# Kernel optimization log

Measured on AMD Instinct MI355X. Metric: run time of the kernel, lower is better.

The kernel has to match this reference:

```python
import jax, jax.numpy as jnp
import numpy as np

B, N_IN, N_H, N_OUT = 128, 256, 256, 256


def _bimul(W, X):
    # MatrixBiMul: bilinear map W X W^T, W: [out, in], X: [b, in, in] -> [b, out, out]
    return jnp.einsum('oi,bij,qj->boq', W, X, W)


def setup_inputs() -> dict:
    key = jax.random.key(0)
    ks = jax.random.split(key, 12)
    s_in = 1.0 / np.sqrt(N_IN)
    s_h = 1.0 / np.sqrt(N_H)
    return {
        'input': jax.random.normal(ks[0], (B, N_IN, N_IN), jnp.float32),
        'hidden': jax.random.normal(ks[1], (B, N_H, N_H), jnp.float32),
        'cell': jax.random.normal(ks[2], (B, N_H, N_H), jnp.float32),
        'W_fx': jax.random.normal(ks[3], (N_H, N_IN), jnp.float32) * s_in,
        'W_ix': jax.random.normal(ks[4], (N_H, N_IN), jnp.float32) * s_in,
        'W_ox': jax.random.normal(ks[5], (N_OUT, N_IN), jnp.float32) * s_in,
        'W_gx': jax.random.normal(ks[6], (N_H, N_IN), jnp.float32) * s_in,
        'W_fh': jax.random.normal(ks[7], (N_H, N_H), jnp.float32) * s_h,
        'W_ih': jax.random.normal(ks[8], (N_H, N_H), jnp.float32) * s_h,
        'W_oh': jax.random.normal(ks[9], (N_OUT, N_H), jnp.float32) * s_h,
        'W_gh': jax.random.normal(ks[10], (N_H, N_H), jnp.float32) * s_h,
        'W_oc': jax.random.normal(ks[11], (N_OUT, N_H), jnp.float32) * s_h,
    }


def reference(input, hidden, cell, W_fx, W_ix, W_ox, W_gx, W_fh, W_ih, W_oh, W_gh, W_oc):
    fgate = jax.nn.relu(_bimul(W_fx, input) + _bimul(W_fh, hidden))
    igate = jax.nn.relu(_bimul(W_ix, input) + _bimul(W_ih, hidden))
    ogate = jax.nn.relu(_bimul(W_ox, input) + _bimul(W_oh, hidden))
    ggate = jax.nn.relu(_bimul(W_gx, input) + _bimul(W_gh, hidden))
    c = fgate + cell + igate + ggate  # note: additive, as in source (not fgate*cell)
    h = ogate + jax.nn.relu(_bimul(W_oc, c))
    return (h, c)
```

## Files before the change

### kernel.cpp

```cpp
#include <hip/hip_runtime.h>

typedef __bf16 bf16x8 __attribute__((ext_vector_type(8)));
typedef float f32x4 __attribute__((ext_vector_type(4)));

__device__ __forceinline__ unsigned short f2bf(float f) {
    unsigned int u = __builtin_bit_cast(unsigned int, f);
    u += 0x7fff + ((u >> 16) & 1);
    return (unsigned short)(u >> 16);
}

__device__ __forceinline__ void stage_tile(
    const unsigned short* __restrict__ Ap, int lda,
    const unsigned short* __restrict__ Bp, int ldb,
    unsigned short* lds, int k0, int tid)
{
#pragma unroll
    for (int it = 0; it < 4; ++it) {
        int li = it * 256 + tid;
        int row = li >> 3;
        int sc = ((li & 7) ^ (row & 7)) * 8;
        __builtin_amdgcn_global_load_lds(
            (const __attribute__((address_space(1))) void*)(Ap + (long)row * lda + k0 + sc),
            (__attribute__((address_space(3))) void*)&lds[li * 8], 16, 0, 0);
        __builtin_amdgcn_global_load_lds(
            (const __attribute__((address_space(1))) void*)(Bp + (long)row * ldb + k0 + sc),
            (__attribute__((address_space(3))) void*)&lds[8192 + li * 8], 16, 0, 0);
    }
}

__device__ __forceinline__ void compute_tile(
    const unsigned short* lds, int lane, int wm, int wn, f32x4 (&acc)[4][4])
{
#pragma unroll
    for (int kk = 0; kk < 2; ++kk) {
        const int cl = kk * 4 + (lane >> 4);
        bf16x8 af[4], bfr[4];
#pragma unroll
        for (int m = 0; m < 4; ++m) {
            int row = wm + m * 16 + (lane & 15);
            af[m] = *(const bf16x8*)&lds[row * 64 + ((cl ^ (row & 7)) * 8)];
        }
#pragma unroll
        for (int n = 0; n < 4; ++n) {
            int row = wn + n * 16 + (lane & 15);
            bfr[n] = *(const bf16x8*)&lds[8192 + row * 64 + ((cl ^ (row & 7)) * 8)];
        }
#pragma unroll
        for (int m = 0; m < 4; ++m)
#pragma unroll
            for (int n = 0; n < 4; ++n)
                acc[m][n] = __builtin_amdgcn_mfma_f32_16x16x32_bf16(af[m], bfr[n], acc[m][n], 0, 0, 0);
    }
}

__global__ __launch_bounds__(256)
void transpose_cvt(const float* __restrict__ S0, unsigned short* __restrict__ D0,
                   const float* __restrict__ S1, unsigned short* __restrict__ D1)
{
    const float* S = blockIdx.z ? S1 : S0;
    unsigned short* D = blockIdx.z ? D1 : D0;
    const int b = blockIdx.y;
    const int t = blockIdx.x;
    const int r0 = (t >> 2) * 64;
    const int c0 = (t & 3) * 64;
    S += (long)b * 65536;
    D += (long)b * 65536;

    __shared__ float tile[64][65];
    const int tid = threadIdx.x;

#pragma unroll
    for (int it = 0; it < 4; ++it) {
        int r = it * 16 + (tid >> 4);
        int c = (tid & 15) * 4;
        float4 v = *(const float4*)&S[(long)(r0 + r) * 256 + c0 + c];
        tile[r][c + 0] = v.x; tile[r][c + 1] = v.y;
        tile[r][c + 2] = v.z; tile[r][c + 3] = v.w;
    }
    __syncthreads();
#pragma unroll
    for (int it = 0; it < 16; ++it) {
        int rr = it * 4 + (tid >> 6);
        int cc = tid & 63;
        D[(long)(c0 + rr) * 256 + r0 + cc] = f2bf(tile[cc][rr]);
    }
}

__global__ __launch_bounds__(256)
void cvt_weights(const float* __restrict__ fx, const float* __restrict__ ix,
                 const float* __restrict__ ox, const float* __restrict__ gx,
                 const float* __restrict__ fh, const float* __restrict__ ih,
                 const float* __restrict__ oh, const float* __restrict__ gh,
                 const float* __restrict__ oc,
                 unsigned short* __restrict__ Wcat, unsigned short* __restrict__ Wocb)
{
    int idx = blockIdx.x * 256 + threadIdx.x;
    if (idx < 524288) {
        int g = idx >> 17;
        int rem = idx & 131071;
        int q = rem >> 9;
        int j = rem & 511;
        const float* xs = (g == 0) ? fx : (g == 1) ? ix : (g == 2) ? ox : gx;
        const float* hs = (g == 0) ? fh : (g == 1) ? ih : (g == 2) ? oh : gh;
        float v = (j < 256) ? xs[q * 256 + j] : hs[q * 256 + (j - 256)];
        Wcat[idx] = f2bf(v);
    } else if (idx < 589824) {
        int k = idx - 524288;
        Wocb[k] = f2bf(oc[k]);
    }
}

__global__ __launch_bounds__(256)
void gemm_stageA(const unsigned short* __restrict__ Wcat,
                 const unsigned short* __restrict__ XbT,
                 const unsigned short* __restrict__ HbT,
                 unsigned short* __restrict__ Tcat)
{
    __shared__ alignas(16) unsigned short lds[32768];

    const int tid = threadIdx.x;
    const int lane = tid & 63;
    const int w = tid >> 6;

    int d = blockIdx.x + 4 * blockIdx.y + 512 * blockIdx.z;
    int swz = (d & 7) * 512 + (d >> 3);
    const int x = swz & 3;
    const int b = (swz >> 2) & 127;
    const int gz = swz >> 9;
    const int g = gz >> 1, hf = gz & 1;
    const int tm = (x >> 1) * 128;
    const int tn = (x & 1) * 128;
    const int wm = (w >> 1) * 64;
    const int wn = (w & 1) * 64;

    const unsigned short* Ap = Wcat + (long)g * 131072 + hf * 256 + (long)tm * 512;
    const unsigned short* Bp = (hf ? HbT : XbT) + (long)b * 65536 + (long)tn * 256;

    f32x4 acc[4][4];
#pragma unroll
    for (int m = 0; m < 4; ++m)
#pragma unroll
        for (int n = 0; n < 4; ++n)
            acc[m][n] = (f32x4){0.f, 0.f, 0.f, 0.f};

    stage_tile(Ap, 512, Bp, 256, lds, 0, tid);
    __syncthreads();
    int cur = 0;
    for (int t = 0; t < 4; ++t) {
        if (t + 1 < 4)
            stage_tile(Ap, 512, Bp, 256, lds + (cur ^ 1) * 16384, (t + 1) * 64, tid);
        compute_tile(lds + cur * 16384, lane, wm, wn, acc);
        __syncthreads();
        cur ^= 1;
    }

    unsigned short* C = Tcat + (long)g * 16777216 + (long)b * 131072 + hf * 256;
    const int r0 = (lane >> 4) * 4;
    const int c0 = lane & 15;
#pragma unroll
    for (int m = 0; m < 4; ++m)
#pragma unroll
        for (int n = 0; n < 4; ++n)
#pragma unroll
            for (int r = 0; r < 4; ++r) {
                int row = tm + wm + m * 16 + r0 + r;
                int col = tn + wn + n * 16 + c0;
                C[(long)row * 512 + col] = f2bf(acc[m][n][r]);
            }
}

__global__ __launch_bounds__(256)
void gemm_gateB(const unsigned short* __restrict__ Tcat,
                const unsigned short* __restrict__ Wcat,
                const float* __restrict__ cell,
                float* __restrict__ out_c, float* __restrict__ out_h,
                unsigned short* __restrict__ CbT)
{
    __shared__ alignas(16) unsigned short lds[32768];

    const int tid = threadIdx.x;
    const int lane = tid & 63;
    const int w = tid >> 6;
    const int zc = (blockIdx.z == 0);

    int orig = blockIdx.x + 4 * blockIdx.y;
    int swz = (orig & 7) * 64 + (orig >> 3);
    const int x = swz & 3;
    const int b = swz >> 2;
    const int tm = (x >> 1) * 128;
    const int tn = (x & 1) * 128;
    const int wm = (w >> 1) * 64;
    const int wn = (w & 1) * 64;

    const int nseg = zc ? 3 : 1;
    auto abase = [&](int seg) -> const unsigned short* {
        int gv = zc ? (seg + (seg >> 1)) : 2;
        return Tcat + (long)gv * 16777216 + (long)b * 131072 + (long)tm * 512;
    };
    auto bbase = [&](int seg) -> const unsigned short* {
        int gv = zc ? (seg + (seg >> 1)) : 2;
        return Wcat + (long)gv * 131072 + (long)tn * 512;
    };

    f32x4 accc[4][4];
#pragma unroll
    for (int m = 0; m < 4; ++m)
#pragma unroll
        for (int n = 0; n < 4; ++n)
            accc[m][n] = (f32x4){0.f, 0.f, 0.f, 0.f};

    stage_tile(abase(0), 512, bbase(0), 512, lds, 0, tid);
    __syncthreads();
    int cur = 0;
    const int nt = nseg * 8;
    for (int seg = 0; seg < nseg; ++seg) {
        f32x4 acc[4][4];
#pragma unroll
        for (int m = 0; m < 4; ++m)
#pragma unroll
            for (int n = 0; n < 4; ++n)
                acc[m][n] = (f32x4){0.f, 0.f, 0.f, 0.f};
        for (int ks = 0; ks < 8; ++ks) {
            int u = seg * 8 + ks;
            if (u + 1 < nt) {
                int s2 = (u + 1) >> 3;
                int k2 = ((u + 1) & 7) * 64;
                stage_tile(abase(s2), 512, bbase(s2), 512, lds + (cur ^ 1) * 16384, k2, tid);
            }
            compute_tile(lds + cur * 16384, lane, wm, wn, acc);
            __syncthreads();
            cur ^= 1;
        }
#pragma unroll
        for (int m = 0; m < 4; ++m)
#pragma unroll
            for (int n = 0; n < 4; ++n)
#pragma unroll
                for (int r = 0; r < 4; ++r) {
                    float v = acc[m][n][r];
                    accc[m][n][r] += (v > 0.f ? v : 0.f);
                }
    }

    const int r0 = (lane >> 4) * 4;
    const int c0 = lane & 15;
    if (zc) {
        unsigned short (*ldsT)[136] = (unsigned short(*)[136])lds;
        const float* cb = cell + (long)b * 65536;
        float* co = out_c + (long)b * 65536;
#pragma unroll
        for (int m = 0; m < 4; ++m)
#pragma unroll
            for (int n = 0; n < 4; ++n)
#pragma unroll
                for (int r = 0; r < 4; ++r) {
                    int row = wm + m * 16 + r0 + r;
                    int col = wn + n * 16 + c0;
                    float v = accc[m][n][r] + cb[(long)(tm + row) * 256 + tn + col];
                    co[(long)(tm + row) * 256 + tn + col] = v;
                    ldsT[col][row] = f2bf(v);
                }
        __syncthreads();
        unsigned short* cbt = CbT + (long)b * 65536;
#pragma unroll
        for (int it = 0; it < 8; ++it) {
            int idx = it * 256 + tid;
            int jj = idx >> 4;
            int ch = idx & 15;
            uint4 v = *(const uint4*)&ldsT[jj][ch * 8];
            *(uint4*)&cbt[(long)(tn + jj) * 256 + tm + ch * 8] = v;
        }
    } else {
        float* ho = out_h + (long)b * 65536;
#pragma unroll
        for (int m = 0; m < 4; ++m)
#pragma unroll
            for (int n = 0; n < 4; ++n)
#pragma unroll
                for (int r = 0; r < 4; ++r) {
                    int row = tm + wm + m * 16 + r0 + r;
                    int col = tn + wn + n * 16 + c0;
                    ho[(long)row * 256 + col] = accc[m][n][r];
                }
    }
}

template <int MODE>
__global__ __launch_bounds__(256)
void gemm_nt2(const unsigned short* __restrict__ A, int lda, long sAy,
              const unsigned short* __restrict__ B, int ldb, long sBy,
              void* __restrict__ Cv, int ldc, long sCy, int nt)
{
    __shared__ alignas(16) unsigned short lds[32768];

    const int tid = threadIdx.x;
    const int lane = tid & 63;
    const int w = tid >> 6;

    int orig = blockIdx.x + 4 * blockIdx.y;
    int swz = (orig & 7) * 64 + (orig >> 3);
    const int x = swz & 3;
    const int b = swz >> 2;
    const int tm = (x >> 1) * 128;
    const int tn = (x & 1) * 128;
    const int wm = (w >> 1) * 64;
    const int wn = (w & 1) * 64;

    const unsigned short* Ap = A + b * sAy + (long)tm * lda;
    const unsigned short* Bp = B + b * sBy + (long)tn * ldb;

    f32x4 acc[4][4];
#pragma unroll
    for (int m = 0; m < 4; ++m)
#pragma unroll
        for (int n = 0; n < 4; ++n)
            acc[m][n] = (f32x4){0.f, 0.f, 0.f, 0.f};

    stage_tile(Ap, lda, Bp, ldb, lds, 0, tid);
    __syncthreads();
    int cur = 0;
    for (int t = 0; t < nt; ++t) {
        if (t + 1 < nt)
            stage_tile(Ap, lda, Bp, ldb, lds + (cur ^ 1) * 16384, (t + 1) * 64, tid);
        compute_tile(lds + cur * 16384, lane, wm, wn, acc);
        __syncthreads();
        cur ^= 1;
    }

    const long coff = b * sCy;
    const int r0 = (lane >> 4) * 4;
    const int c0 = lane & 15;

    if (MODE == 0) {
        unsigned short* C = (unsigned short*)Cv + coff;
#pragma unroll
        for (int m = 0; m < 4; ++m)
#pragma unroll
            for (int n = 0; n < 4; ++n)
#pragma unroll
                for (int r = 0; r < 4; ++r) {
                    int row = tm + wm + m * 16 + r0 + r;
                    int col = tn + wn + n * 16 + c0;
                    C[(long)row * ldc + col] = f2bf(acc[m][n][r]);
                }
    } else {
        float* C = (float*)Cv + coff;
#pragma unroll
        for (int m = 0; m < 4; ++m)
#pragma unroll
            for (int n = 0; n < 4; ++n)
#pragma unroll
                for (int r = 0; r < 4; ++r) {
                    int row = tm + wm + m * 16 + r0 + r;
                    int col = tn + wn + n * 16 + c0;
                    long idx = (long)row * ldc + col;
                    float v = acc[m][n][r];
                    C[idx] += (v > 0.f ? v : 0.f);
                }
    }
}

extern "C" void kernel_launch(void* const* d_in, const int* in_sizes, int n_in,
                              void* d_out, int out_size, void* d_ws, size_t ws_size,
                              hipStream_t stream)
{
    (void)in_sizes; (void)n_in; (void)out_size; (void)ws_size;

    const float* X    = (const float*)d_in[0];
    const float* H    = (const float*)d_in[1];
    const float* cell = (const float*)d_in[2];
    const float* Wxp[4] = {(const float*)d_in[3], (const float*)d_in[4],
                           (const float*)d_in[5], (const float*)d_in[6]};
    const float* Whp[4] = {(const float*)d_in[7], (const float*)d_in[8],
                           (const float*)d_in[9], (const float*)d_in[10]};
    const float* Wocf = (const float*)d_in[11];

    float* out_h = (float*)d_out;
    float* out_c = out_h + 8388608;

    unsigned short* ws   = (unsigned short*)d_ws;
    unsigned short* XbT  = ws;
    unsigned short* HbT  = ws + 8388608;
    unsigned short* Wcat = ws + 16777216;
    unsigned short* Wocb = ws + 17301504;
    unsigned short* Tcat = ws + 17367040;
    unsigned short* CbT  = XbT;
    unsigned short* U    = HbT;

    transpose_cvt<<<dim3(16, 128, 2), 256, 0, stream>>>(X, XbT, H, HbT);
    cvt_weights<<<dim3(2304), 256, 0, stream>>>(Wxp[0], Wxp[1], Wxp[2], Wxp[3],
                                                Whp[0], Whp[1], Whp[2], Whp[3],
                                                Wocf, Wcat, Wocb);
    gemm_stageA<<<dim3(4, 128, 8), 256, 0, stream>>>(Wcat, XbT, HbT, Tcat);
    gemm_gateB<<<dim3(4, 128, 2), 256, 0, stream>>>(Tcat, Wcat, cell, out_c, out_h, CbT);
    gemm_nt2<0><<<dim3(4, 128), 256, 0, stream>>>(
        Wocb, 256, 0L, CbT, 256, 65536L,
        (void*)U, 256, 65536L, 4);
    gemm_nt2<2><<<dim3(4, 128), 256, 0, stream>>>(
        U, 256, 65536L, Wocb, 256, 0L,
        (void*)out_h, 256, 65536L, 4);
}
```

Baseline: 194.4 us.

## Fuse fp32-to-bf16 transpose into first GEMM stage and single-buffer LDS

Drops the separate transpose/convert kernel. The first-stage GEMM now reads fp32 X/H directly, converts them to bf16 in registers and writes them into LDS, and its output goes through an LDS transpose so global stores are coalesced. The gate kernel no longer writes a bf16 transposed copy of c. Instead, the final stage re-reads fp32 out_c through the same fused-convert GEMM. GEMMs switch from double-buffered to single-buffered LDS, which cuts shared memory use and may raise occupancy, but loads no longer overlap with compute.

Result: slower. 203.6 us (+4.7%).

```diff
diff --git a/kernel.cpp b/kernel.cpp
--- a/kernel.cpp
+++ b/kernel.cpp
@@ -50,39 +50,6 @@
 #pragma unroll
             for (int n = 0; n < 4; ++n)
                 acc[m][n] = __builtin_amdgcn_mfma_f32_16x16x32_bf16(af[m], bfr[n], acc[m][n], 0, 0, 0);
-    }
-}
-
-__global__ __launch_bounds__(256)
-void transpose_cvt(const float* __restrict__ S0, unsigned short* __restrict__ D0,
-                   const float* __restrict__ S1, unsigned short* __restrict__ D1)
-{
-    const float* S = blockIdx.z ? S1 : S0;
-    unsigned short* D = blockIdx.z ? D1 : D0;
-    const int b = blockIdx.y;
-    const int t = blockIdx.x;
-    const int r0 = (t >> 2) * 64;
-    const int c0 = (t & 3) * 64;
-    S += (long)b * 65536;
-    D += (long)b * 65536;
-
-    __shared__ float tile[64][65];
-    const int tid = threadIdx.x;
-
-#pragma unroll
-    for (int it = 0; it < 4; ++it) {
-        int r = it * 16 + (tid >> 4);
-        int c = (tid & 15) * 4;
-        float4 v = *(const float4*)&S[(long)(r0 + r) * 256 + c0 + c];
-        tile[r][c + 0] = v.x; tile[r][c + 1] = v.y;
-        tile[r][c + 2] = v.z; tile[r][c + 3] = v.w;
-    }
-    __syncthreads();
-#pragma unroll
-    for (int it = 0; it < 16; ++it) {
-        int rr = it * 4 + (tid >> 6);
-        int cc = tid & 63;
-        D[(long)(c0 + rr) * 256 + r0 + cc] = f2bf(tile[cc][rr]);
     }
 }
 
@@ -110,31 +77,35 @@
     }
 }
 
+template <int MODE>
 __global__ __launch_bounds__(256)
-void gemm_stageA(const unsigned short* __restrict__ Wcat,
-                 const unsigned short* __restrict__ XbT,
-                 const unsigned short* __restrict__ HbT,
-                 unsigned short* __restrict__ Tcat)
-{
-    __shared__ alignas(16) unsigned short lds[32768];
+void gemm_stage1(const float* __restrict__ Xf, const float* __restrict__ Hf,
+                 const unsigned short* __restrict__ Wb,
+                 unsigned short* __restrict__ Tout)
+{
+    __shared__ alignas(16) unsigned short lds[17408];
 
     const int tid = threadIdx.x;
     const int lane = tid & 63;
     const int w = tid >> 6;
 
     int d = blockIdx.x + 4 * blockIdx.y + 512 * blockIdx.z;
-    int swz = (d & 7) * 512 + (d >> 3);
+    int swz = (MODE == 0) ? ((d & 7) * 512 + (d >> 3))
+                          : ((d & 7) * 64 + (d >> 3));
     const int x = swz & 3;
     const int b = (swz >> 2) & 127;
-    const int gz = swz >> 9;
+    const int gz = (MODE == 0) ? (swz >> 9) : 0;
     const int g = gz >> 1, hf = gz & 1;
-    const int tm = (x >> 1) * 128;
-    const int tn = (x & 1) * 128;
+    const int ti = (x & 1) * 128;
+    const int tq = (x >> 1) * 128;
     const int wm = (w >> 1) * 64;
     const int wn = (w & 1) * 64;
-
-    const unsigned short* Ap = Wcat + (long)g * 131072 + hf * 256 + (long)tm * 512;
-    const unsigned short* Bp = (hf ? HbT : XbT) + (long)b * 65536 + (long)tn * 256;
+    const int ldb = (MODE == 0) ? 512 : 256;
+
+    const float* Ap = ((MODE == 0) ? (hf ? Hf : Xf) : Xf) + (long)b * 65536 + (long)ti * 256;
+    const unsigned short* Bp = (MODE == 0)
+        ? Wb + (long)g * 131072 + (long)tq * 512 + hf * 256
+        : Wb + (long)tq * 256;
 
     f32x4 acc[4][4];
 #pragma unroll
@@ -143,18 +114,58 @@
         for (int n = 0; n < 4; ++n)
             acc[m][n] = (f32x4){0.f, 0.f, 0.f, 0.f};
 
-    stage_tile(Ap, 512, Bp, 256, lds, 0, tid);
+    float4 pre[4][2];
+#pragma unroll
+    for (int it = 0; it < 4; ++it) {
+        int li = it * 256 + tid;
+        int row = li >> 3;
+        int ck = li & 7;
+        const float* ga = Ap + (long)row * 256 + ck * 8;
+        pre[it][0] = *(const float4*)ga;
+        pre[it][1] = *(const float4*)(ga + 4);
+    }
+
+    for (int t = 0; t < 4; ++t) {
+        if (t > 0) __syncthreads();
+#pragma unroll
+        for (int it = 0; it < 4; ++it) {
+            int li = it * 256 + tid;
+            int row = li >> 3;
+            int sc = ((li & 7) ^ (row & 7)) * 8;
+            __builtin_amdgcn_global_load_lds(
+                (const __attribute__((address_space(1))) void*)(Bp + (long)row * ldb + t * 64 + sc),
+                (__attribute__((address_space(3))) void*)&lds[8192 + li * 8], 16, 0, 0);
+        }
+#pragma unroll
+        for (int it = 0; it < 4; ++it) {
+            int li = it * 256 + tid;
+            int row = li >> 3;
+            int ck = li & 7;
+            const float* pf = (const float*)&pre[it][0];
+            uint4 uv;
+            uv.x = (unsigned)f2bf(pf[0]) | ((unsigned)f2bf(pf[1]) << 16);
+            uv.y = (unsigned)f2bf(pf[2]) | ((unsigned)f2bf(pf[3]) << 16);
+            uv.z = (unsigned)f2bf(pf[4]) | ((unsigned)f2bf(pf[5]) << 16);
+            uv.w = (unsigned)f2bf(pf[6]) | ((unsigned)f2bf(pf[7]) << 16);
+            *(uint4*)&lds[row * 64 + ((ck ^ (row & 7)) * 8)] = uv;
+        }
+        __syncthreads();
+        if (t < 3) {
+#pragma unroll
+            for (int it = 0; it < 4; ++it) {
+                int li = it * 256 + tid;
+                int row = li >> 3;
+                int ck = li & 7;
+                const float* ga = Ap + (long)row * 256 + (t + 1) * 64 + ck * 8;
+                pre[it][0] = *(const float4*)ga;
+                pre[it][1] = *(const float4*)(ga + 4);
+            }
+        }
+        compute_tile(lds, lane, wm, wn, acc);
+    }
+
     __syncthreads();
-    int cur = 0;
-    for (int t = 0; t < 4; ++t) {
-        if (t + 1 < 4)
-            stage_tile(Ap, 512, Bp, 256, lds + (cur ^ 1) * 16384, (t + 1) * 64, tid);
-        compute_tile(lds + cur * 16384, lane, wm, wn, acc);
-        __syncthreads();
-        cur ^= 1;
-    }
-
-    unsigned short* C = Tcat + (long)g * 16777216 + (long)b * 131072 + hf * 256;
+    unsigned short (*ldsT)[136] = (unsigned short(*)[136])lds;
     const int r0 = (lane >> 4) * 4;
     const int c0 = lane & 15;
 #pragma unroll
@@ -163,20 +174,32 @@
         for (int n = 0; n < 4; ++n)
 #pragma unroll
             for (int r = 0; r < 4; ++r) {
-                int row = tm + wm + m * 16 + r0 + r;
-                int col = tn + wn + n * 16 + c0;
-                C[(long)row * 512 + col] = f2bf(acc[m][n][r]);
+                int row = wm + m * 16 + r0 + r;
+                int col = wn + n * 16 + c0;
+                ldsT[col][row] = f2bf(acc[m][n][r]);
             }
+    __syncthreads();
+    unsigned short* Cb;
+    int ldc;
+    if (MODE == 0) { Cb = Tout + (long)g * 16777216 + (long)b * 131072 + hf * 256; ldc = 512; }
+    else           { Cb = Tout + (long)b * 65536; ldc = 256; }
+#pragma unroll
+    for (int it = 0; it < 8; ++it) {
+        int idx = it * 256 + tid;
+        int qq = idx >> 4;
+        int ch = idx & 15;
+        uint4 v = *(const uint4*)&ldsT[qq][ch * 8];
+        *(uint4*)&Cb[(long)(tq + qq) * ldc + ti + ch * 8] = v;
+    }
 }
 
 __global__ __launch_bounds__(256)
 void gemm_gateB(const unsigned short* __restrict__ Tcat,
                 const unsigned short* __restrict__ Wcat,
                 const float* __restrict__ cell,
-                float* __restrict__ out_c, float* __restrict__ out_h,
-                unsigned short* __restrict__ CbT)
-{
-    __shared__ alignas(16) unsigned short lds[32768];
+                float* __restrict__ out_c, float* __restrict__ out_h)
+{
+    __shared__ alignas(16) unsigned short lds[16384];
 
     const int tid = threadIdx.x;
     const int lane = tid & 63;
@@ -187,33 +210,24 @@
     int swz = (orig & 7) * 64 + (orig >> 3);
     const int x = swz & 3;
     const int b = swz >> 2;
-    const int tm = (x >> 1) * 128;
-    const int tn = (x & 1) * 128;
+    const int to = (x >> 1) * 128;
+    const int tq = (x & 1) * 128;
     const int wm = (w >> 1) * 64;
     const int wn = (w & 1) * 64;
 
     const int nseg = zc ? 3 : 1;
-    auto abase = [&](int seg) -> const unsigned short* {
+
+    f32x4 accc[4][4];
+#pragma unroll
+    for (int m = 0; m < 4; ++m)
+#pragma unroll
+        for (int n = 0; n < 4; ++n)
+            accc[m][n] = (f32x4){0.f, 0.f, 0.f, 0.f};
+
+    for (int seg = 0; seg < nseg; ++seg) {
         int gv = zc ? (seg + (seg >> 1)) : 2;
-        return Tcat + (long)gv * 16777216 + (long)b * 131072 + (long)tm * 512;
-    };
-    auto bbase = [&](int seg) -> const unsigned short* {
-        int gv = zc ? (seg + (seg >> 1)) : 2;
-        return Wcat + (long)gv * 131072 + (long)tn * 512;
-    };
-
-    f32x4 accc[4][4];
-#pragma unroll
-    for (int m = 0; m < 4; ++m)
-#pragma unroll
-        for (int n = 0; n < 4; ++n)
-            accc[m][n] = (f32x4){0.f, 0.f, 0.f, 0.f};
-
-    stage_tile(abase(0), 512, bbase(0), 512, lds, 0, tid);
-    __syncthreads();
-    int cur = 0;
-    const int nt = nseg * 8;
-    for (int seg = 0; seg < nseg; ++seg) {
+        const unsigned short* Ap = Wcat + (long)gv * 131072 + (long)to * 512;
+        const unsigned short* Bp = Tcat + (long)gv * 16777216 + (long)b * 131072 + (long)tq * 512;
         f32x4 acc[4][4];
 #pragma unroll
         for (int m = 0; m < 4; ++m)
@@ -221,15 +235,10 @@
             for (int n = 0; n < 4; ++n)
                 acc[m][n] = (f32x4){0.f, 0.f, 0.f, 0.f};
         for (int ks = 0; ks < 8; ++ks) {
-            int u = seg * 8 + ks;
-            if (u + 1 < nt) {
-                int s2 = (u + 1) >> 3;
-                int k2 = ((u + 1) & 7) * 64;
-                stage_tile(abase(s2), 512, bbase(s2), 512, lds + (cur ^ 1) * 16384, k2, tid);
-            }
-            compute_tile(lds + cur * 16384, lane, wm, wn, acc);
+            if (seg + ks > 0) __syncthreads();
+            stage_tile(Ap, 512, Bp, 512, lds, ks * 64, tid);
             __syncthreads();
-            cur ^= 1;
+            compute_tile(lds, lane, wm, wn, acc);
         }
 #pragma unroll
         for (int m = 0; m < 4; ++m)
@@ -245,7 +254,6 @@
     const int r0 = (lane >> 4) * 4;
     const int c0 = lane & 15;
     if (zc) {
-        unsigned short (*ldsT)[136] = (unsigned short(*)[136])lds;
         const float* cb = cell + (long)b * 65536;
         float* co = out_c + (long)b * 65536;
 #pragma unroll
@@ -254,22 +262,10 @@
             for (int n = 0; n < 4; ++n)
 #pragma unroll
                 for (int r = 0; r < 4; ++r) {
-                    int row = wm + m * 16 + r0 + r;
-                    int col = wn + n * 16 + c0;
-                    float v = accc[m][n][r] + cb[(long)(tm + row) * 256 + tn + col];
-                    co[(long)(tm + row) * 256 + tn + col] = v;
-                    ldsT[col][row] = f2bf(v);
+                    int row = to + wm + m * 16 + r0 + r;
+                    int col = tq + wn + n * 16 + c0;
+                    co[(long)row * 256 + col] = accc[m][n][r] + cb[(long)row * 256 + col];
                 }
-        __syncthreads();
-        unsigned short* cbt = CbT + (long)b * 65536;
-#pragma unroll
-        for (int it = 0; it < 8; ++it) {
-            int idx = it * 256 + tid;
-            int jj = idx >> 4;
-            int ch = idx & 15;
-            uint4 v = *(const uint4*)&ldsT[jj][ch * 8];
-            *(uint4*)&cbt[(long)(tn + jj) * 256 + tm + ch * 8] = v;
-        }
     } else {
         float* ho = out_h + (long)b * 65536;
 #pragma unroll
@@ -278,20 +274,19 @@
             for (int n = 0; n < 4; ++n)
 #pragma unroll
                 for (int r = 0; r < 4; ++r) {
-                    int row = tm + wm + m * 16 + r0 + r;
-                    int col = tn + wn + n * 16 + c0;
+                    int row = to + wm + m * 16 + r0 + r;
+                    int col = tq + wn + n * 16 + c0;
                     ho[(long)row * 256 + col] = accc[m][n][r];
                 }
     }
 }
 
-template <int MODE>
 __global__ __launch_bounds__(256)
-void gemm_nt2(const unsigned short* __restrict__ A, int lda, long sAy,
-              const unsigned short* __restrict__ B, int ldb, long sBy,
-              void* __restrict__ Cv, int ldc, long sCy, int nt)
-{
-    __shared__ alignas(16) unsigned short lds[32768];
+void gemm_hfinal(const unsigned short* __restrict__ Wocb,
+                 const unsigned short* __restrict__ ScT,
+                 float* __restrict__ out_h)
+{
+    __shared__ alignas(16) unsigned short lds[16384];
 
     const int tid = threadIdx.x;
     const int lane = tid & 63;
@@ -301,13 +296,13 @@
     int swz = (orig & 7) * 64 + (orig >> 3);
     const int x = swz & 3;
     const int b = swz >> 2;
-    const int tm = (x >> 1) * 128;
-    const int tn = (x & 1) * 128;
+    const int to = (x >> 1) * 128;
+    const int tq = (x & 1) * 128;
     const int wm = (w >> 1) * 64;
     const int wn = (w & 1) * 64;
 
-    const unsigned short* Ap = A + b * sAy + (long)tm * lda;
-    const unsigned short* Bp = B + b * sBy + (long)tn * ldb;
+    const unsigned short* Ap = Wocb + (long)to * 256;
+    const unsigned short* Bp = ScT + (long)b * 65536 + (long)tq * 256;
 
     f32x4 acc[4][4];
 #pragma unroll
@@ -316,48 +311,27 @@
         for (int n = 0; n < 4; ++n)
             acc[m][n] = (f32x4){0.f, 0.f, 0.f, 0.f};
 
-    stage_tile(Ap, lda, Bp, ldb, lds, 0, tid);
-    __syncthreads();
-    int cur = 0;
-    for (int t = 0; t < nt; ++t) {
-        if (t + 1 < nt)
-            stage_tile(Ap, lda, Bp, ldb, lds + (cur ^ 1) * 16384, (t + 1) * 64, tid);
-        compute_tile(lds + cur * 16384, lane, wm, wn, acc);
+    for (int t = 0; t < 4; ++t) {
+        if (t > 0) __syncthreads();
+        stage_tile(Ap, 256, Bp, 256, lds, t * 64, tid);
         __syncthreads();
-        cur ^= 1;
-    }
-
-    const long coff = b * sCy;
+        compute_tile(lds, lane, wm, wn, acc);
+    }
+
+    float* ho = out_h + (long)b * 65536;
     const int r0 = (lane >> 4) * 4;
     const int c0 = lane & 15;
-
-    if (MODE == 0) {
-        unsigned short* C = (unsigned short*)Cv + coff;
-#pragma unroll
-        for (int m = 0; m < 4; ++m)
-#pragma unroll
-            for (int n = 0; n < 4; ++n)
-#pragma unroll
-                for (int r = 0; r < 4; ++r) {
-                    int row = tm + wm + m * 16 + r0 + r;
-                    int col = tn + wn + n * 16 + c0;
-                    C[(long)row * ldc + col] = f2bf(acc[m][n][r]);
-                }
-    } else {
-        float* C = (float*)Cv + coff;
-#pragma unroll
-        for (int m = 0; m < 4; ++m)
-#pragma unroll
-            for (int n = 0; n < 4; ++n)
-#pragma unroll
-                for (int r = 0; r < 4; ++r) {
-                    int row = tm + wm + m * 16 + r0 + r;
-                    int col = tn + wn + n * 16 + c0;
-                    long idx = (long)row * ldc + col;
-                    float v = acc[m][n][r];
-                    C[idx] += (v > 0.f ? v : 0.f);
-                }
-    }
+#pragma unroll
+    for (int m = 0; m < 4; ++m)
+#pragma unroll
+        for (int n = 0; n < 4; ++n)
+#pragma unroll
+            for (int r = 0; r < 4; ++r) {
+                int row = to + wm + m * 16 + r0 + r;
+                int col = tq + wn + n * 16 + c0;
+                float v = acc[m][n][r];
+                ho[(long)row * 256 + col] += (v > 0.f ? v : 0.f);
+            }
 }
 
 extern "C" void kernel_launch(void* const* d_in, const int* in_sizes, int n_in,
@@ -379,24 +353,16 @@
     float* out_c = out_h + 8388608;
 
     unsigned short* ws   = (unsigned short*)d_ws;
-    unsigned short* XbT  = ws;
-    unsigned short* HbT  = ws + 8388608;
+    unsigned short* ScT  = ws;
     unsigned short* Wcat = ws + 16777216;
     unsigned short* Wocb = ws + 17301504;
     unsigned short* Tcat = ws + 17367040;
-    unsigned short* CbT  = XbT;
-    unsigned short* U    = HbT;
-
-    transpose_cvt<<<dim3(16, 128, 2), 256, 0, stream>>>(X, XbT, H, HbT);
+
     cvt_weights<<<dim3(2304), 256, 0, stream>>>(Wxp[0], Wxp[1], Wxp[2], Wxp[3],
                                                 Whp[0], Whp[1], Whp[2], Whp[3],
                                                 Wocf, Wcat, Wocb);
-    gemm_stageA<<<dim3(4, 128, 8), 256, 0, stream>>>(Wcat, XbT, HbT, Tcat);
-    gemm_gateB<<<dim3(4, 128, 2), 256, 0, stream>>>(Tcat, Wcat, cell, out_c, out_h, CbT);
-    gemm_nt2<0><<<dim3(4, 128), 256, 0, stream>>>(
-        Wocb, 256, 0L, CbT, 256, 65536L,
-        (void*)U, 256, 65536L, 4);
-    gemm_nt2<2><<<dim3(4, 128), 256, 0, stream>>>(
-        U, 256, 65536L, Wocb, 256, 0L,
-        (void*)out_h, 256, 65536L, 4);
-}
+    gemm_stage1<0><<<dim3(4, 128, 8), 256, 0, stream>>>(X, H, Wcat, Tcat);
+    gemm_gateB<<<dim3(4, 128, 2), 256, 0, stream>>>(Tcat, Wcat, cell, out_c, out_h);
+    gemm_stage1<1><<<dim3(4, 128, 1), 256, 0, stream>>>(out_c, nullptr, Wocb, ScT);
+    gemm_hfinal<<<dim3(4, 128), 256, 0, stream>>>(Wocb, ScT, out_h);
+}
```
